# Optimization experiments

Hardware: AMD Instinct MI355X
Metric: run time of the kernel (lower is better)

The kernel has to match this reference:

```python
import jax, jax.numpy as jnp
import numpy as np
import math

PHI = (1.0 + math.sqrt(5.0)) / 2.0
ALPHA = 0.01
I_ROT = math.pi / 2.0
B, IN, H = 4096, 1024, 1024
GIN = IN + 4 * H  # input + 2H (h flat) + 2H (surfaced flat)


def _mag(z):
    return jnp.sqrt(z[..., 0] ** 2 + z[..., 1] ** 2 + 1e-8)


def _phase(z):
    return jnp.arctan2(z[..., 1], z[..., 0] + 1e-10)


@jax.custom_vjp
def fractal_compress(mag):
    m = jnp.maximum(mag, 1e-8)
    return m ** (2.0 / 3.0)


def _fc_fwd(mag):
    m = jnp.maximum(mag, 1e-8)
    c = m ** (2.0 / 3.0)
    return c, c / (m + 1e-6)


def _fc_bwd(ratio, g):
    return (g * jnp.minimum(ratio, 2.0),)


fractal_compress.defvjp(_fc_fwd, _fc_bwd)


def converge(z):
    mag = _mag(z)
    ph = _phase(z)
    cm = fractal_compress(mag)
    return jnp.stack([cm * jnp.cos(ph), cm * jnp.sin(ph)], axis=-1)


def resonance_gate(a, b):
    d = _phase(a) - _phase(b)
    return jnp.cos(d / 2.0) ** 2


def _uni(k, shape, fan_in):
    s = (1.0 / PHI) / math.sqrt(fan_in)
    return jax.random.uniform(k, shape, jnp.float32, -s, s)


def setup_inputs() -> dict:
    key = jax.random.key(0)
    ks = jax.random.split(key, 12)
    return {
        "x_t": jax.random.normal(ks[0], (B, IN), jnp.float32),
        "h_prev": jax.random.normal(ks[1], (B, H, 2), jnp.float32),
        "c_prev": jax.random.normal(ks[2], (B, H, 2), jnp.float32),
        "d_prev": jax.random.normal(ks[3], (B, H, 2), jnp.float32),
        "b_prev": jax.random.uniform(ks[4], (B, 1), jnp.float32),
        "Wf_w": _uni(ks[5], (H, GIN), GIN), "Wf_b": jnp.zeros((H,), jnp.float32),
        "Wi_w": _uni(ks[6], (H, GIN), GIN), "Wi_b": jnp.zeros((H,), jnp.float32),
        "Wo_w": _uni(ks[7], (H, GIN), GIN), "Wo_b": jnp.zeros((H,), jnp.float32),
        "Wc_w": _uni(ks[8], (2 * H, GIN), GIN), "Wc_b": jnp.zeros((2 * H,), jnp.float32),
        "Wr_w": _uni(ks[9], (2 * H, IN), IN), "Wr_b": jnp.zeros((2 * H,), jnp.float32),
        "theta": jnp.full((H,), I_ROT, jnp.float32),
    }


def reference(x_t, h_prev, c_prev, d_prev, b_prev,
              Wf_w, Wf_b, Wi_w, Wi_b, Wo_w, Wo_b, Wc_w, Wc_b, Wr_w, Wr_b, theta):
    batch = x_t.shape[0]
    hid = theta.shape[0]

    # boundary: real input -> complex
    x_complex = (x_t @ Wr_w.T + Wr_b).reshape(batch, hid, 2)

    # memory surfacing from the (detached) worldline
    d_read = jax.lax.stop_gradient(d_prev)
    T = resonance_gate(x_complex, d_read)                      # (B, H)
    d_mag = _mag(d_read)[..., None]                            # (B, H, 1)
    d_normed = d_read / (d_mag + 1e-8)
    d_scale = jnp.sqrt(jnp.clip(d_mag, 1e-6, 20.0))
    surfaced = d_normed * d_scale * T[..., None]               # (B, H, 2)

    combined = jnp.concatenate(
        [x_t, h_prev.reshape(batch, -1), surfaced.reshape(batch, -1)], axis=-1)

    f_raw = combined @ Wf_w.T + Wf_b
    i_raw = combined @ Wi_w.T + Wi_b
    o_raw = combined @ Wo_w.T + Wo_b

    temperature = (2.0 * b_prev + 1e-4)[..., None]             # (B, 1, 1)
    gate_stack = jnp.stack([f_raw, i_raw, o_raw], axis=-1)     # (B, H, 3)
    gw = jax.nn.softmax(gate_stack / temperature, axis=-1)
    f_t, i_t, o_t = gw[..., 0], gw[..., 1], gw[..., 2]

    g_raw = combined @ Wc_w.T + Wc_b
    g_t = jnp.stack([jnp.tanh(g_raw[:, :hid]), jnp.tanh(g_raw[:, hid:])], axis=-1)

    # convergence: released surface -> fractal-compressed -> worldline
    released = (1.0 - f_t)[..., None] * c_prev
    compressed = jnp.clip(converge(released), -10.0, 10.0)
    d_t = jax.lax.stop_gradient(d_prev) + ALPHA * compressed
    d_mag_new = _mag(d_t)[..., None]
    d_t = jnp.where(d_mag_new > 20.0, d_t * (20.0 / d_mag_new), d_t)

    # cell update + i-rotation
    c_updated = f_t[..., None] * c_prev + i_t[..., None] * g_t
    cos_t = jnp.cos(theta)[None, :, None]
    sin_t = jnp.sin(theta)[None, :, None]
    cr, ci = c_updated[..., 0:1], c_updated[..., 1:2]
    c_t = jnp.concatenate([cos_t * cr - sin_t * ci, sin_t * cr + cos_t * ci], axis=-1)

    c_squashed = jnp.stack([jnp.tanh(c_t[..., 0]), jnp.tanh(c_t[..., 1])], axis=-1)
    h_raw = o_t[..., None] * c_squashed
    G = resonance_gate(h_raw, d_t)
    h_t = G[..., None] * h_raw

    # balance update from energy split
    conv_e = (_mag(released) ** 2).sum(axis=-1, keepdims=True)
    emer_e = (_mag(h_t) ** 2).sum(axis=-1, keepdims=True)
    b_measured = conv_e / (conv_e + emer_e + 1e-8)
    b_t = 0.99 * b_prev + 0.01 * b_measured

    h_t = jnp.nan_to_num(h_t, nan=0.0)
    c_t = jnp.nan_to_num(c_t, nan=0.0)
    d_t = jnp.nan_to_num(d_t, nan=0.0)
    b_t = jnp.nan_to_num(b_t, nan=0.5)
    return (h_t, c_t, d_t, b_t)
```

## Files before the change

### kernel.cpp

```cpp
#include <hip/hip_runtime.h>
#include <math.h>

typedef unsigned short u16;
typedef unsigned int u32;
typedef u16 u16x4 __attribute__((ext_vector_type(4)));
typedef float f32x2 __attribute__((ext_vector_type(2)));
typedef float f32x4 __attribute__((ext_vector_type(4)));
typedef __bf16 bf16x8 __attribute__((ext_vector_type(8)));

__device__ __forceinline__ u16 f2bf(float f){
  u32 u = __builtin_bit_cast(u32, f);
  u32 r = u + 0x7FFFu + ((u >> 16) & 1u);
  return (u16)(r >> 16);
}
__device__ __forceinline__ float bf2f(u16 h){
  u32 u = ((u32)h) << 16;
  return __builtin_bit_cast(float, u);
}
__device__ __forceinline__ float ftanh(float x){
  float e = __expf(2.f*x);
  return 1.f - 2.f/(e+1.f);
}

typedef __attribute__((address_space(1))) const unsigned int gas_u32;
typedef __attribute__((address_space(3))) unsigned int las_u32;
__device__ __forceinline__ void gload_lds16(const void* g, void* l){
  __builtin_amdgcn_global_load_lds((gas_u32*)g, (las_u32*)l, 16, 0, 0);
}

__global__ __launch_bounds__(256) void cvt_hi(const float* __restrict__ in, u16* __restrict__ out, int n4){
  int i = blockIdx.x*256 + threadIdx.x;
  if (i >= n4) return;
  f32x4 v = *(const f32x4*)(in + (size_t)i*4);
  u16x4 o;
  #pragma unroll
  for (int j=0;j<4;++j) o[j]=f2bf(v[j]);
  *(u16x4*)(out + (size_t)i*4) = o;
}

__global__ __launch_bounds__(256) void cvt_hilo(const float* __restrict__ in, u16* __restrict__ hi, u16* __restrict__ lo, int n4){
  int i = blockIdx.x*256 + threadIdx.x;
  if (i >= n4) return;
  f32x4 v = *(const f32x4*)(in + (size_t)i*4);
  u16x4 oh, ol;
  #pragma unroll
  for (int j=0;j<4;++j){ u16 h=f2bf(v[j]); oh[j]=h; ol[j]=f2bf(v[j]-bf2f(h)); }
  *(u16x4*)(hi + (size_t)i*4) = oh;
  *(u16x4*)(lo + (size_t)i*4) = ol;
}

__global__ __launch_bounds__(256) void cvt_xh(const float* __restrict__ x, const float* __restrict__ h,
                                              u16* __restrict__ cA, u16* __restrict__ xlo){
  int b = blockIdx.y;
  int c0 = (blockIdx.x*256 + threadIdx.x)*4;
  f32x4 v;
  if (c0 < 1024) v = *(const f32x4*)(x + (size_t)b*1024 + c0);
  else           v = *(const f32x4*)(h + (size_t)b*2048 + (c0-1024));
  u16x4 hi4;
  #pragma unroll
  for (int j=0;j<4;++j) hi4[j]=f2bf(v[j]);
  *(u16x4*)(cA + (size_t)b*5120 + c0) = hi4;
  if (c0 < 1024){
    u16x4 lo4;
    #pragma unroll
    for (int j=0;j<4;++j) lo4[j]=f2bf(v[j]-bf2f(hi4[j]));
    *(u16x4*)(xlo + (size_t)b*1024 + c0) = lo4;
  }
}

__global__ __launch_bounds__(256) void prep_surf(const float* __restrict__ xc, const float* __restrict__ dp,
                                                 const int* __restrict__ smap, float* __restrict__ Scmp,
                                                 u16* __restrict__ cA, int cap){
  int i = blockIdx.x*256 + threadIdx.x;
  int b = i >> 10, h = i & 1023;
  f32x2 z = *(const f32x2*)(xc + 2*(size_t)i);
  f32x2 d = *(const f32x2*)(dp + 2*(size_t)i);
  float zx = z[0] + 1e-10f, dx = d[0] + 1e-10f;
  float hz = sqrtf(zx*zx + z[1]*z[1]);
  float hd = sqrtf(dx*dx + d[1]*d[1]);
  float cosd = (zx*dx + z[1]*d[1]) / fmaxf(hz*hd, 1e-30f);
  float T = 0.5f + 0.5f*cosd;
  float dmag = sqrtf(d[0]*d[0] + d[1]*d[1] + 1e-8f);
  float dscale = sqrtf(fminf(fmaxf(dmag, 1e-6f), 20.0f));
  float s = T * dscale / (dmag + 1e-8f);
  float o0 = d[0]*s, o1 = d[1]*s;
  u32 pk = (u32)f2bf(o0) | ((u32)f2bf(o1) << 16);
  *(u32*)&cA[(size_t)b*5120 + 3072 + 2*h] = pk;
  int p = smap[b];
  if (p >= 0 && p < cap)
    *(f32x2*)(Scmp + ((size_t)p*1024 + h)*2) = f32x2{o0, o1};
}

__global__ __launch_bounds__(256) void flag_rows(const float* __restrict__ bp, int* __restrict__ out,
                                                 int* __restrict__ smap, int cap){
  __shared__ int cnt;
  if (threadIdx.x==0) cnt=0;
  __syncthreads();
  for (int i=threadIdx.x; i<4096; i+=256){
    int p = -1;
    if (bp[i] < 0.04f){
      p = atomicAdd(&cnt,1);
      if (p < cap) out[1+p]=i;
    }
    smap[i] = p;
  }
  __syncthreads();
  if (threadIdx.x==0) out[0] = min(cnt, cap);
}

__global__ __launch_bounds__(256) void fix_init(const int* __restrict__ smap, const int* __restrict__ cr,
    const float* __restrict__ b0, const float* __restrict__ b1, const float* __restrict__ b2,
    float* __restrict__ C){
  int b = blockIdx.x;
  int p = smap[b];
  if (p < 0 || p >= cr[0]) return;
  #pragma unroll
  for (int j0=0; j0<3072; j0+=256){
    int j = j0 + threadIdx.x;
    float bb = (j<1024) ? b0[j] : ((j<2048) ? b1[j-1024] : b2[j-2048]);
    C[(size_t)b*3072 + j] = bb;
  }
}

template<bool SPLIT, bool OUTBF, int NB>
__global__ __launch_bounds__(256) void gemm_fast(
    const u16* __restrict__ Ah, int lda,
    const u16* __restrict__ Al, int ldal,
    const u16* __restrict__ Bh, int ldb,
    const u16* __restrict__ Bl,
    const float* __restrict__ bias0, const float* __restrict__ bias1, const float* __restrict__ bias2,
    float* __restrict__ Cf, u16* __restrict__ Cb, int ldc, int K)
{
  __shared__ u16 sAh[128*32];
  __shared__ u16 sBh[128*32];
  __shared__ u16 sAl[SPLIT?128*32:8];
  __shared__ u16 sBl[SPLIT?128*32:8];

  const int tid=threadIdx.x, lane=tid&63, w=tid>>6;

  const int gx = gridDim.x;
  const int nwg = gx * gridDim.y;
  const int lin = blockIdx.y*gx + blockIdx.x;
  const int sw = (lin & 7)*(nwg >> 3) + (lin >> 3);
  const int m0 = (sw / gx)*128, n0 = (sw % gx)*128;

  const int wm=(w>>1), wn=w&1, l16=lane&15, hi16=lane>>4;

  const int c0=(w*2+0)*64+lane, c1=c0+64;
  const int r0=c0>>2, sp0=(c0&3)^(r0&3);
  const int r1=c1>>2, sp1=(c1&3)^(r1&3);
  u16* lA0 = sAh + (w*2+0)*512; u16* lA1 = sAh + (w*2+1)*512;
  u16* lB0 = sBh + (w*2+0)*512; u16* lB1 = sBh + (w*2+1)*512;
  const u16* A0 = Ah + (size_t)(m0+r0)*lda + sp0*8;
  const u16* A1 = Ah + (size_t)(m0+r1)*lda + sp1*8;
  const u16* B0 = Bh + (size_t)(n0+r0)*ldb + sp0*8;
  const u16* B1 = Bh + (size_t)(n0+r1)*ldb + sp1*8;
  const u16 *A0l=nullptr,*A1l=nullptr,*B0l=nullptr,*B1l=nullptr;
  u16 *lA0l=nullptr,*lA1l=nullptr,*lB0l=nullptr,*lB1l=nullptr;
  if constexpr(SPLIT){
    A0l = Al + (size_t)(m0+r0)*ldal + sp0*8;
    A1l = Al + (size_t)(m0+r1)*ldal + sp1*8;
    B0l = Bl + (size_t)(n0+r0)*ldb  + sp0*8;
    B1l = Bl + (size_t)(n0+r1)*ldb  + sp1*8;
    lA0l = sAl + (w*2+0)*512; lA1l = sAl + (w*2+1)*512;
    lB0l = sBl + (w*2+0)*512; lB1l = sBl + (w*2+1)*512;
  }

  const int axor = (hi16 ^ (l16&3))*8;
  const int aoff = (wm*64 + l16)*32 + axor;
  const int boff = (wn*64 + l16)*32 + axor;

  f32x4 acc[4][4];
  #pragma unroll
  for (int a=0;a<4;++a)
    #pragma unroll
    for (int b=0;b<4;++b) acc[a][b] = f32x4{0.f,0.f,0.f,0.f};

  for (int k0=0; k0<K; k0+=32){
    gload_lds16(A0+k0, lA0);
    gload_lds16(A1+k0, lA1);
    gload_lds16(B0+k0, lB0);
    gload_lds16(B1+k0, lB1);
    if constexpr(SPLIT){
      gload_lds16(A0l+k0, lA0l);
      gload_lds16(A1l+k0, lA1l);
      gload_lds16(B0l+k0, lB0l);
      gload_lds16(B1l+k0, lB1l);
    }
    __syncthreads();
    bf16x8 fa[4], fb[4], fal[4], fbl[4];
    #pragma unroll
    for (int f=0; f<4; ++f){
      fa[f] = *(const bf16x8*)&sAh[aoff + f*512];
      fb[f] = *(const bf16x8*)&sBh[boff + f*512];
      if constexpr(SPLIT){
        fal[f] = *(const bf16x8*)&sAl[aoff + f*512];
        fbl[f] = *(const bf16x8*)&sBl[boff + f*512];
      }
    }
    #pragma unroll
    for (int fm=0; fm<4; ++fm){
      #pragma unroll
      for (int fn=0; fn<4; ++fn){
        acc[fm][fn] = __builtin_amdgcn_mfma_f32_16x16x32_bf16(fa[fm], fb[fn], acc[fm][fn], 0,0,0);
        if constexpr(SPLIT){
          acc[fm][fn] = __builtin_amdgcn_mfma_f32_16x16x32_bf16(fal[fm], fb[fn],  acc[fm][fn], 0,0,0);
          acc[fm][fn] = __builtin_amdgcn_mfma_f32_16x16x32_bf16(fa[fm],  fbl[fn], acc[fm][fn], 0,0,0);
        }
      }
    }
    __syncthreads();
  }

  #pragma unroll
  for (int fm=0; fm<4; ++fm){
    int grow = m0 + wm*64 + fm*16 + hi16*4;
    #pragma unroll
    for (int fn=0; fn<4; ++fn){
      int gcol = n0 + wn*64 + fn*16 + l16;
      float bb;
      if constexpr(NB==3) bb = (gcol<1024) ? bias0[gcol] : ((gcol<2048) ? bias1[gcol-1024] : bias2[gcol-2048]);
      else bb = bias0[gcol];
      #pragma unroll
      for (int r2=0;r2<4;++r2){
        float v = acc[fm][fn][r2] + bb;
        if constexpr(OUTBF) Cb[(size_t)(grow+r2)*ldc + gcol] = f2bf(v);
        else                Cf[(size_t)(grow+r2)*ldc + gcol] = v;
      }
    }
  }
}

#define LSTR 40
#define FIX_KC 8
#define FIX_KLEN 640
__global__ __launch_bounds__(256) void gemm_fix_sk(
    const float* __restrict__ Xs, const float* __restrict__ Hs,
    const float* __restrict__ Scmp, const int* __restrict__ smap,
    const float* __restrict__ W0, const float* __restrict__ W1, const float* __restrict__ W2,
    const int* __restrict__ cr, float* __restrict__ C)
{
  const int count = cr[0];
  const int m0 = blockIdx.y * 128;
  if (m0 >= count) return;
  const int* rows = cr + 1;
  const int kbeg = blockIdx.z * FIX_KLEN;
  const int kend = kbeg + FIX_KLEN;

  __shared__ u16 sAh[128*LSTR];
  __shared__ u16 sAl[128*LSTR];
  __shared__ u16 sBh[128*LSTR];
  __shared__ u16 sBl[128*LSTR];

  const int tid = threadIdx.x;
  const int n0 = blockIdx.x * 128;
  int seg = n0 >> 10;
  const float* W = (seg==0) ? W0 : (seg==1 ? W1 : W2);
  int nw = n0 & 1023;

  const int wave = tid >> 6, lane = tid & 63;
  const int wm = wave >> 1, wn = wave & 1;
  const int l16 = lane & 15, lk8 = (lane >> 4) * 8;

  f32x4 acc[4][4];
  #pragma unroll
  for (int a=0;a<4;++a)
    #pragma unroll
    for (int b=0;b<4;++b) acc[a][b] = f32x4{0.f,0.f,0.f,0.f};

  for (int k0 = kbeg; k0 < kend; k0 += 32){
    #pragma unroll
    for (int i=0;i<4;++i){
      int flat = tid + i*256;
      int r  = flat >> 3;
      int c4 = flat & 7;
      int kk = k0 + c4*4;
      int mrow = rows[min(m0 + r, count-1)];
      const float* srcA;
      if (kk < 1024)      srcA = Xs + (size_t)mrow*1024 + kk;
      else if (kk < 3072) srcA = Hs + (size_t)mrow*2048 + (kk - 1024);
      else                srcA = Scmp + (size_t)smap[mrow]*2048 + (kk - 3072);
      f32x4 va = *(const f32x4*)srcA;
      f32x4 vb = *(const f32x4*)(W + (size_t)(nw + r)*5120 + kk);
      u16x4 ah, bh, al, bl;
      #pragma unroll
      for (int j=0;j<4;++j){
        u16 hA = f2bf(va[j]); ah[j] = hA; al[j] = f2bf(va[j] - bf2f(hA));
        u16 hB = f2bf(vb[j]); bh[j] = hB; bl[j] = f2bf(vb[j] - bf2f(hB));
      }
      int o = r*LSTR + c4*4;
      *(u16x4*)&sAh[o] = ah;
      *(u16x4*)&sBh[o] = bh;
      *(u16x4*)&sAl[o] = al;
      *(u16x4*)&sBl[o] = bl;
    }
    __syncthreads();
    bf16x8 fah[4], fbh[4], fal[4], fbl[4];
    #pragma unroll
    for (int f=0; f<4; ++f){
      int ra  = (wm*64 + f*16 + l16)*LSTR + lk8;
      int rb2 = (wn*64 + f*16 + l16)*LSTR + lk8;
      fah[f] = *(const bf16x8*)&sAh[ra];
      fbh[f] = *(const bf16x8*)&sBh[rb2];
      fal[f] = *(const bf16x8*)&sAl[ra];
      fbl[f] = *(const bf16x8*)&sBl[rb2];
    }
    #pragma unroll
    for (int fm=0; fm<4; ++fm){
      #pragma unroll
      for (int fn=0; fn<4; ++fn){
        acc[fm][fn] = __builtin_amdgcn_mfma_f32_16x16x32_bf16(fah[fm], fbh[fn], acc[fm][fn], 0,0,0);
        acc[fm][fn] = __builtin_amdgcn_mfma_f32_16x16x32_bf16(fal[fm], fbh[fn], acc[fm][fn], 0,0,0);
        acc[fm][fn] = __builtin_amdgcn_mfma_f32_16x16x32_bf16(fah[fm], fbl[fn], acc[fm][fn], 0,0,0);
      }
    }
    __syncthreads();
  }

  #pragma unroll
  for (int fm=0; fm<4; ++fm){
    int trow = wm*64 + fm*16 + (lane>>4)*4;
    #pragma unroll
    for (int fn=0; fn<4; ++fn){
      int lcol = wn*64 + fn*16 + l16;
      #pragma unroll
      for (int r2=0;r2<4;++r2){
        int mi = m0 + trow + r2;
        if (mi < count){
          int mrow = rows[mi];
          atomicAdd(&C[(size_t)mrow*3072 + (n0 + lcol)], acc[fm][fn][r2]);
        }
      }
    }
  }
}

__global__ __launch_bounds__(256) void epilogue(
    const float* __restrict__ rawfio, const u16* __restrict__ rawg,
    const float* __restrict__ c_prev, const float* __restrict__ d_prev,
    const float* __restrict__ b_prev, const float* __restrict__ theta,
    float* __restrict__ out)
{
  const int b = blockIdx.x;
  const int tid = threadIdx.x;
  float* Hout = out;
  float* Cout = out + (size_t)8388608;
  float* Dout = out + (size_t)16777216;
  float* Bout = out + (size_t)25165824;
  const float bp = b_prev[b];
  const float inv_t = 1.0f / (2.0f*bp + 1e-4f);
  float conv_acc = 0.f, emer_acc = 0.f;
  const size_t rb3 = (size_t)b*3072;
  const size_t rg = (size_t)b*2048;

  #pragma unroll
  for (int j=0;j<4;++j){
    int h = tid + j*256;
    float fr = rawfio[rb3 + h];
    float ir = rawfio[rb3 + 1024 + h];
    float og = rawfio[rb3 + 2048 + h];
    float g0 = bf2f(rawg[rg + h]);
    float g1 = bf2f(rawg[rg + 1024 + h]);

    float mx = fmaxf(fr, fmaxf(ir, og));
    float ef = __expf((fr-mx)*inv_t);
    float ei = __expf((ir-mx)*inv_t);
    float eo = __expf((og-mx)*inv_t);
    float inv_s = 1.0f/(ef+ei+eo);
    float ft = ef*inv_s, it = ei*inv_s, ot = eo*inv_s;

    f32x2 cp = *(const f32x2*)(c_prev + 2*((size_t)b*1024 + h));
    f32x2 dp = *(const f32x2*)(d_prev + 2*((size_t)b*1024 + h));

    float r0 = (1.f-ft)*cp[0], r1 = (1.f-ft)*cp[1];
    float rm2 = r0*r0 + r1*r1;
    conv_acc += rm2 + 1e-8f;
    float rmag = sqrtf(rm2 + 1e-8f);
    float cm = __expf(0.66666667f * __logf(rmag));
    float rx = r0 + 1e-10f;
    float hr = fmaxf(sqrtf(rx*rx + r1*r1), 1e-30f);
    float invhr = cm / hr;
    float comp0 = fminf(fmaxf(rx*invhr, -10.f), 10.f);
    float comp1 = fminf(fmaxf(r1*invhr, -10.f), 10.f);

    float d0 = dp[0] + 0.01f*comp0;
    float d1 = dp[1] + 0.01f*comp1;
    float dmn = sqrtf(d0*d0 + d1*d1 + 1e-8f);
    if (dmn > 20.f){ float sc = 20.f/dmn; d0*=sc; d1*=sc; }

    float gt0 = ftanh(g0), gt1 = ftanh(g1);
    float cu0 = ft*cp[0] + it*gt0;
    float cu1 = ft*cp[1] + it*gt1;
    float th = theta[h];
    float sth, cth;
    __sincosf(th, &sth, &cth);
    float c0 = cth*cu0 - sth*cu1;
    float c1 = sth*cu0 + cth*cu1;
    float cs0 = ftanh(c0), cs1 = ftanh(c1);
    float hr0 = ot*cs0, hr1 = ot*cs1;

    float hx = hr0 + 1e-10f, dx = d0 + 1e-10f;
    float hh = sqrtf(hx*hx + hr1*hr1);
    float hd = sqrtf(dx*dx + d1*d1);
    float cosd = (hx*dx + hr1*d1) / fmaxf(hh*hd, 1e-30f);
    float G = 0.5f + 0.5f*cosd;
    float h0 = G*hr0, h1 = G*hr1;
    emer_acc += h0*h0 + h1*h1 + 1e-8f;

    h0 = (h0==h0)?h0:0.f;  h1 = (h1==h1)?h1:0.f;
    c0 = (c0==c0)?c0:0.f;  c1 = (c1==c1)?c1:0.f;
    d0 = (d0==d0)?d0:0.f;  d1 = (d1==d1)?d1:0.f;

    size_t oi = 2*((size_t)b*1024 + h);
    *(f32x2*)(Hout+oi) = f32x2{h0,h1};
    *(f32x2*)(Cout+oi) = f32x2{c0,c1};
    *(f32x2*)(Dout+oi) = f32x2{d0,d1};
  }

  #pragma unroll
  for (int off=32; off; off>>=1){
    conv_acc += __shfl_down(conv_acc, off);
    emer_acc += __shfl_down(emer_acc, off);
  }
  __shared__ float sred[8];
  int wv = tid>>6, ln = tid&63;
  if (ln==0){ sred[wv]=conv_acc; sred[4+wv]=emer_acc; }
  __syncthreads();
  if (tid==0){
    float cv = sred[0]+sred[1]+sred[2]+sred[3];
    float em = sred[4]+sred[5]+sred[6]+sred[7];
    float bm = cv/(cv+em+1e-8f);
    float bt = 0.99f*bp + 0.01f*bm;
    bt = (bt==bt)?bt:0.5f;
    Bout[b] = bt;
  }
}

extern "C" void kernel_launch(void* const* d_in, const int* in_sizes, int n_in,
                              void* d_out, int out_size, void* d_ws, size_t ws_size,
                              hipStream_t stream)
{
  const float* x_t    = (const float*)d_in[0];
  const float* h_prev = (const float*)d_in[1];
  const float* c_prev = (const float*)d_in[2];
  const float* d_prev = (const float*)d_in[3];
  const float* b_prev = (const float*)d_in[4];
  const float* Wf_w   = (const float*)d_in[5];
  const float* Wf_b   = (const float*)d_in[6];
  const float* Wi_w   = (const float*)d_in[7];
  const float* Wi_b   = (const float*)d_in[8];
  const float* Wo_w   = (const float*)d_in[9];
  const float* Wo_b   = (const float*)d_in[10];
  const float* Wc_w   = (const float*)d_in[11];
  const float* Wc_b   = (const float*)d_in[12];
  const float* Wr_w   = (const float*)d_in[13];
  const float* Wr_b   = (const float*)d_in[14];
  const float* theta  = (const float*)d_in[15];

  char* W = (char*)d_ws;
  float* rawfio = (float*)W;
  float* xc     = (float*)W;
  u16*   Wr_hi  = (u16*)(W + 50331648);
  u16*   Wr_lo  = (u16*)(W + 50331648 + 4194304);
  u16*   x_lo   = (u16*)(W + 50331648 + 8388608);
  u16*   raw_g  = (u16*)(W + 50331648);
  u16*   cA     = (u16*)(W + 67108864);
  u16*   WD     = (u16*)(W + 109051904);
  int*   idx    = (int*)(W + 140509184);
  int*   smap   = (int*)(W + 140509184 + 16388);
  float* Scmp   = (float*)(W + 140546048);
  long long avail = (long long)ws_size - 140546048LL;
  int cap = (int)(avail > 0 ? avail / 8192 : 0);
  if (cap > 1024) cap = 1024;

  dim3 blk(256);

  cvt_xh<<<dim3(3,4096), blk, 0, stream>>>(x_t, h_prev, cA, x_lo);
  cvt_hilo<<<2048, blk, 0, stream>>>(Wr_w, Wr_hi, Wr_lo, 524288);
  gemm_fast<true,false,1><<<dim3(16,32), blk, 0, stream>>>(
      cA, 5120, x_lo, 1024, Wr_hi, 1024, Wr_lo,
      Wr_b, nullptr, nullptr, xc, nullptr, 2048, 1024);
  flag_rows<<<1, blk, 0, stream>>>(b_prev, idx, smap, cap);
  prep_surf<<<16384, blk, 0, stream>>>(xc, d_prev, smap, Scmp, cA, cap);
  cvt_hi<<<5120, blk, 0, stream>>>(Wf_w, WD, 1310720);
  cvt_hi<<<5120, blk, 0, stream>>>(Wi_w, WD + (size_t)1024*5120, 1310720);
  cvt_hi<<<5120, blk, 0, stream>>>(Wo_w, WD + (size_t)2048*5120, 1310720);
  gemm_fast<false,false,3><<<dim3(24,32), blk, 0, stream>>>(
      cA, 5120, nullptr, 0, WD, 5120, nullptr,
      Wf_b, Wi_b, Wo_b, rawfio, nullptr, 3072, 5120);
  fix_init<<<4096, blk, 0, stream>>>(smap, idx, Wf_b, Wi_b, Wo_b, rawfio);
  gemm_fix_sk<<<dim3(24,8,FIX_KC), blk, 0, stream>>>(
      x_t, h_prev, Scmp, smap, Wf_w, Wi_w, Wo_w, idx, rawfio);
  cvt_hi<<<10240, blk, 0, stream>>>(Wc_w, WD, 2621440);
  gemm_fast<false,true,1><<<dim3(16,32), blk, 0, stream>>>(
      cA, 5120, nullptr, 0, WD, 5120, nullptr,
      Wc_b, nullptr, nullptr, nullptr, raw_g, 2048, 5120);
  epilogue<<<4096, blk, 0, stream>>>(rawfio, raw_g, c_prev, d_prev, b_prev, theta, (float*)d_out);
}
```

Measured before the change: 571.5 us.

## Add 8-wave 256-row GEMM with phased LDS double-buffering for gate GEMMs

Introduces a new 512-thread GEMM kernel that computes 256xBN tiles with eight waves. It uses direct global-to-LDS loads, swizzled LDS, a two-stage ping-pong pipeline split into eight phases, setprio around MFMA bursts and a grid swizzle that spreads work across XCDs. It replaces the 128x128 bf16 kernel for the f/i/o and candidate GEMMs, aiming for more data reuse per tile and better overlap of loads with MFMA. The cost is higher register and LDS pressure, fewer workgroups, and fragile hand-scheduled barriers.

After: 527.2 us. 7.8% less time.

```diff
diff --git a/kernel.cpp b/kernel.cpp
--- a/kernel.cpp
+++ b/kernel.cpp
@@ -119,6 +119,121 @@
     int j = j0 + threadIdx.x;
     float bb = (j<1024) ? b0[j] : ((j<2048) ? b1[j-1024] : b2[j-2048]);
     C[(size_t)b*3072 + j] = bb;
+  }
+}
+
+#define LDA8(BUF,H,MH,J) (*(const bf16x8*)(sAc + ((BUF)*2+(H))*16384 + abase + (MH)*4096 + (J)*1024))
+#define LDB8(BUF,H,N)    (*(const bf16x8*)(sBc + ((BUF)*2+(H))*BHTB + bbase + (N)*1024))
+#define STG_A8(BUF,H,TT) { const u16* s_ = Ah + aS + (size_t)(TT)*64 + (H)*32; \
+    gload_lds16(s_, dA + ((BUF)*2+(H))*8192); \
+    gload_lds16(s_ + aS2, dA + ((BUF)*2+(H))*8192 + 4096); }
+#define STG_B8(BUF,H,TT) { const u16* s_ = Bh + bS + (size_t)(TT)*64 + (H)*32; \
+    gload_lds16(s_, dB + ((BUF)*2+(H))*(BHTB/2)); \
+    if constexpr (NR==4){ gload_lds16(s_ + bS2, dB + ((BUF)*2+(H))*(BHTB/2) + 4096); } }
+#define PH8(BUF,H,MH,RB,STG,DOW) do{ \
+    bf16x8 af0 = LDA8(BUF,H,MH,0), af1 = LDA8(BUF,H,MH,1), af2 = LDA8(BUF,H,MH,2), af3 = LDA8(BUF,H,MH,3); \
+    if (RB){ _Pragma("unroll") for(int n_=0;n_<NR;++n_) bfr[n_] = LDB8(BUF,H,n_); } \
+    STG; \
+    asm volatile("" ::: "memory"); \
+    __builtin_amdgcn_s_barrier(); \
+    asm volatile("s_waitcnt lgkmcnt(0)" ::: "memory"); \
+    __builtin_amdgcn_sched_barrier(0); \
+    __builtin_amdgcn_s_setprio(1); \
+    _Pragma("unroll") for(int n_=0;n_<NR;++n_){ \
+      acc[(MH)*4+0][n_] = __builtin_amdgcn_mfma_f32_16x16x32_bf16(af0, bfr[n_], acc[(MH)*4+0][n_],0,0,0); \
+      acc[(MH)*4+1][n_] = __builtin_amdgcn_mfma_f32_16x16x32_bf16(af1, bfr[n_], acc[(MH)*4+1][n_],0,0,0); \
+      acc[(MH)*4+2][n_] = __builtin_amdgcn_mfma_f32_16x16x32_bf16(af2, bfr[n_], acc[(MH)*4+2][n_],0,0,0); \
+      acc[(MH)*4+3][n_] = __builtin_amdgcn_mfma_f32_16x16x32_bf16(af3, bfr[n_], acc[(MH)*4+3][n_],0,0,0); } \
+    __builtin_amdgcn_s_setprio(0); \
+    if (DOW) { asm volatile("s_waitcnt vmcnt(%0)" :: "i"(VN) : "memory"); } \
+    asm volatile("" ::: "memory"); \
+    __builtin_amdgcn_s_barrier(); \
+    __builtin_amdgcn_sched_barrier(0); \
+  }while(0)
+
+template<int NR, bool OUTBF, int NB>
+__global__ __launch_bounds__(512) void gemm8p(
+    const u16* __restrict__ Ah, int lda,
+    const u16* __restrict__ Bh, int ldb,
+    const float* __restrict__ bias0, const float* __restrict__ bias1, const float* __restrict__ bias2,
+    float* __restrict__ Cf, u16* __restrict__ Cb, int ldc, int K)
+{
+  constexpr int BN   = NR*64;
+  constexpr int BHTB = BN*64;
+  constexpr int VN   = (NR==4) ? 4 : 3;
+  __shared__ u16 sA[4*8192];
+  __shared__ u16 sB[4*(NR*2048)];
+  const char* sAc = (const char*)sA;
+  const char* sBc = (const char*)sB;
+
+  const int tid = threadIdx.x, lane = tid&63, w8 = tid>>6;
+  const int wr = w8>>2, wc = w8&3;
+  const int l16 = lane&15;
+
+  const int gx = gridDim.x, nwg = gx*gridDim.y;
+  const int lin = blockIdx.y*gx + blockIdx.x;
+  const int sw = (lin&7)*(nwg>>3) + (lin>>3);
+  const int m0 = (sw / gx)*256, n0 = (sw % gx)*BN;
+
+  const int rowS  = tid>>2;
+  const int ksS   = (tid&3) ^ ((tid>>3)&3);
+  const size_t aS = (size_t)(m0 + rowS)*lda + ksS*8;
+  const size_t aS2= (size_t)128*lda;
+  const size_t bS = (size_t)(n0 + rowS)*ldb + ksS*8;
+  const size_t bS2= (size_t)128*ldb;
+  u16* dA = sA + w8*512;
+  u16* dB = sB + w8*512;
+
+  const int aslot = (lane>>4) ^ ((l16>>1)&3);
+  const int abase = (wr*128 + l16)*64 + aslot*16;
+  const int bbase = (wc*(NR*16) + l16)*64 + aslot*16;
+
+  f32x4 acc[8][NR];
+  #pragma unroll
+  for (int a=0;a<8;++a)
+    #pragma unroll
+    for (int b=0;b<NR;++b) acc[a][b] = f32x4{0.f,0.f,0.f,0.f};
+  bf16x8 bfr[NR];
+
+  const int NT = K>>6, NITER = K>>7;
+
+  STG_A8(0,0,0) STG_B8(0,0,0) STG_A8(0,1,0) STG_B8(0,1,0) STG_A8(1,0,1) STG_B8(1,0,1)
+  asm volatile("s_waitcnt vmcnt(%0)" :: "i"(VN) : "memory");
+  asm volatile("" ::: "memory");
+  __builtin_amdgcn_s_barrier();
+  __builtin_amdgcn_sched_barrier(0);
+
+  for (int i=0; i<NITER; ++i){
+    const int t1 = 2*i+1;
+    const int ta = min(2*i+2, NT-1);
+    const int tb = min(2*i+3, NT-1);
+    PH8(0,0,0,true,  STG_A8(1,1,t1), false);
+    PH8(0,0,1,false, STG_B8(1,1,t1), false);
+    PH8(0,1,0,true,  STG_A8(0,0,ta), false);
+    PH8(0,1,1,false, STG_B8(0,0,ta), true);
+    PH8(1,0,0,true,  STG_A8(0,1,ta), false);
+    PH8(1,0,1,false, STG_B8(0,1,ta), false);
+    PH8(1,1,0,true,  STG_A8(1,0,tb), false);
+    PH8(1,1,1,false, STG_B8(1,0,tb), true);
+  }
+  asm volatile("s_waitcnt vmcnt(0)" ::: "memory");
+
+  #pragma unroll
+  for (int mf=0; mf<8; ++mf){
+    int grow = m0 + wr*128 + mf*16 + (lane>>4)*4;
+    #pragma unroll
+    for (int n=0; n<NR; ++n){
+      int gcol = n0 + wc*(NR*16) + n*16 + l16;
+      float bb;
+      if constexpr(NB==3) bb = (gcol<1024) ? bias0[gcol] : ((gcol<2048) ? bias1[gcol-1024] : bias2[gcol-2048]);
+      else bb = bias0[gcol];
+      #pragma unroll
+      for (int r2=0;r2<4;++r2){
+        float v = acc[mf][n][r2] + bb;
+        if constexpr(OUTBF) Cb[(size_t)(grow+r2)*ldc + gcol] = f2bf(v);
+        else                Cf[(size_t)(grow+r2)*ldc + gcol] = v;
+      }
+    }
   }
 }
 
@@ -485,15 +600,13 @@
   cvt_hi<<<5120, blk, 0, stream>>>(Wf_w, WD, 1310720);
   cvt_hi<<<5120, blk, 0, stream>>>(Wi_w, WD + (size_t)1024*5120, 1310720);
   cvt_hi<<<5120, blk, 0, stream>>>(Wo_w, WD + (size_t)2048*5120, 1310720);
-  gemm_fast<false,false,3><<<dim3(24,32), blk, 0, stream>>>(
-      cA, 5120, nullptr, 0, WD, 5120, nullptr,
-      Wf_b, Wi_b, Wo_b, rawfio, nullptr, 3072, 5120);
+  gemm8p<4,false,3><<<dim3(12,16), dim3(512), 0, stream>>>(
+      cA, 5120, WD, 5120, Wf_b, Wi_b, Wo_b, rawfio, nullptr, 3072, 5120);
   fix_init<<<4096, blk, 0, stream>>>(smap, idx, Wf_b, Wi_b, Wo_b, rawfio);
   gemm_fix_sk<<<dim3(24,8,FIX_KC), blk, 0, stream>>>(
       x_t, h_prev, Scmp, smap, Wf_w, Wi_w, Wo_w, idx, rawfio);
   cvt_hi<<<10240, blk, 0, stream>>>(Wc_w, WD, 2621440);
-  gemm_fast<false,true,1><<<dim3(16,32), blk, 0, stream>>>(
-      cA, 5120, nullptr, 0, WD, 5120, nullptr,
-      Wc_b, nullptr, nullptr, nullptr, raw_g, 2048, 5120);
+  gemm8p<2,true,1><<<dim3(16,16), dim3(512), 0, stream>>>(
+      cA, 5120, WD, 5120, Wc_b, nullptr, nullptr, nullptr, raw_g, 2048, 5120);
   epilogue<<<4096, blk, 0, stream>>>(rawfio, raw_g, c_prev, d_prev, b_prev, theta, (float*)d_out);
 }
```
